# Performance work log

Measured on AMD Instinct MI355X. Metric: run time of the kernel, lower is better.

Reference implementation:

```python
import jax, jax.numpy as jnp
import numpy as np

B, N, DIM = 8, 4096, 512
HEADS, DHEAD = 8, 64
HIDDEN = HEADS * DHEAD  # 512
COND = 512
EPS = 1e-5


def layer_norm(x, gamma, beta):
    mu = jnp.mean(x, axis=-1, keepdims=True)
    var = jnp.var(x, axis=-1, keepdims=True)
    return (x - mu) * jax.lax.rsqrt(var + EPS) * gamma + beta


def setup_inputs() -> dict:
    key = jax.random.key(0)
    ks = jax.random.split(key, 8)
    s_in = 1.0 / np.sqrt(DIM)
    s_cond = 1.0 / np.sqrt(COND)
    s_hid = 1.0 / np.sqrt(HIDDEN)
    return {
        "x": jax.random.normal(ks[0], (B, N, DIM), jnp.float32),
        "conditioning_embeddings": jax.random.normal(ks[1], (B, COND), jnp.float32),
        "gamma_in": jnp.ones((DIM,), jnp.float32),
        "w_cond": jax.random.normal(ks[2], (2 * DIM, COND), jnp.float32) * s_cond,
        "b_cond": jax.random.normal(ks[3], (2 * DIM,), jnp.float32) * 0.01,
        "w_qkv": jax.random.normal(ks[4], (3 * HIDDEN, DIM), jnp.float32) * s_in,
        "w_out": jax.random.normal(ks[5], (DIM, HIDDEN), jnp.float32) * s_hid,
        "gamma_out": jnp.ones((DIM,), jnp.float32),
    }


def reference(x, conditioning_embeddings, gamma_in, w_cond, b_cond, w_qkv, w_out, gamma_out):
    scale_f = DHEAD ** (-0.5)
    # pre-norm
    x = layer_norm(x, gamma_in, jnp.zeros_like(gamma_in))
    # conditioning affine: SiLU -> Linear -> broadcast over tokens
    cond = jax.nn.silu(conditioning_embeddings) @ w_cond.T + b_cond  # [b, 2*dim]
    scale, shift = jnp.split(cond, 2, axis=-1)
    x = x * (scale[:, None, :] + 1.0) + shift[:, None, :]
    # qkv projection (no bias)
    qkv = x @ w_qkv.T  # [b, n, 3*hidden]
    q, k, v = jnp.split(qkv, 3, axis=-1)
    def to_heads(t):
        return t.reshape(B, N, HEADS, DHEAD).transpose(0, 2, 1, 3)  # b h n d
    q, k, v = to_heads(q), to_heads(k), to_heads(v)
    q = jax.nn.softmax(q, axis=-1) * scale_f  # softmax over feature dim
    k = jax.nn.softmax(k, axis=-2)            # softmax over sequence dim
    context = jnp.einsum('bhnd,bhne->bhde', k, v)
    out = jnp.einsum('bhde,bhnd->bhne', context, q)
    out = out.transpose(0, 2, 1, 3).reshape(B, N, HIDDEN)  # b n (h d)
    out = out @ w_out.T
    return layer_norm(out, gamma_out, jnp.zeros_like(gamma_out))
```

## Files before the change

### kernel.cpp

```cpp
#include <hip/hip_runtime.h>
#include <hip/hip_bf16.h>
#include <math.h>

typedef unsigned short u16;
typedef __attribute__((ext_vector_type(4))) float f32x4;
typedef __attribute__((ext_vector_type(8))) short s16x8;

#define B_    8
#define N_    4096
#define DIM_  512
#define TOK   32768
#define QKVD  1536

__device__ __forceinline__ float bf2f(u16 u) {
    union { unsigned int i; float f; } x; x.i = ((unsigned int)u) << 16; return x.f;
}
__device__ __forceinline__ u16 f2bf(float f) {
    union { float f; unsigned int i; } x; x.f = f;
    unsigned int r = (x.i + 0x7fffu + ((x.i >> 16) & 1u)) >> 16;
    return (u16)r;
}

__device__ __forceinline__ void gload_lds16(const void* g, void* l) {
    __builtin_amdgcn_global_load_lds(
        (const __attribute__((address_space(1))) unsigned int*)g,
        (__attribute__((address_space(3))) unsigned int*)l, 16, 0, 0);
}

__device__ __forceinline__ int swz8(int row, int p) { return p ^ (row & 7); }

__global__ void k_cond(const float* __restrict__ ce, const float* __restrict__ w_cond,
                       const float* __restrict__ b_cond, float* __restrict__ cond)
{
    __shared__ float s[512];
    int jt = blockIdx.x, b = blockIdx.y;
    int tid = threadIdx.x, wid = tid >> 6, lane = tid & 63;
    for (int i = tid; i < 512; i += 256) {
        float v = ce[b * 512 + i];
        s[i] = v / (1.f + __expf(-v));
    }
    __syncthreads();
#pragma unroll
    for (int jj = 0; jj < 4; ++jj) {
        int j = jt * 16 + wid * 4 + jj;
        const float4* w4 = (const float4*)(w_cond + (size_t)j * 512);
        float4 a = w4[lane * 2], c = w4[lane * 2 + 1];
        float acc = a.x*s[lane*8+0] + a.y*s[lane*8+1] + a.z*s[lane*8+2] + a.w*s[lane*8+3]
                  + c.x*s[lane*8+4] + c.y*s[lane*8+5] + c.z*s[lane*8+6] + c.w*s[lane*8+7];
#pragma unroll
        for (int d = 1; d < 64; d <<= 1) acc += __shfl_xor(acc, d, 64);
        if (lane == 0) cond[b * 1024 + j] = acc + b_cond[j];
    }
}

__global__ void k_w2bf(const float* __restrict__ w, u16* __restrict__ wb)
{
    int i = (blockIdx.x * 256 + threadIdx.x) * 4;
    float4 v = *(const float4*)&w[i];
    ushort4 o; o.x = f2bf(v.x); o.y = f2bf(v.y); o.z = f2bf(v.z); o.w = f2bf(v.w);
    *(ushort4*)&wb[i] = o;
}

__global__ void k_lnmod(const float* __restrict__ x, const float* __restrict__ cond,
                        const float* __restrict__ gamma, u16* __restrict__ xm)
{
    int wave = threadIdx.x >> 6, lane = threadIdx.x & 63;
    size_t t = (size_t)blockIdx.x * 4 + wave;
    const float* xr = x + t * 512;
    float4 v0 = ((const float4*)xr)[lane * 2];
    float4 v1 = ((const float4*)xr)[lane * 2 + 1];
    float s  = v0.x+v0.y+v0.z+v0.w + v1.x+v1.y+v1.z+v1.w;
    float ss = v0.x*v0.x+v0.y*v0.y+v0.z*v0.z+v0.w*v0.w
             + v1.x*v1.x+v1.y*v1.y+v1.z*v1.z+v1.w*v1.w;
#pragma unroll
    for (int m = 1; m < 64; m <<= 1) { s += __shfl_xor(s, m, 64); ss += __shfl_xor(ss, m, 64); }
    float mu = s * (1.f/512.f);
    float var = ss * (1.f/512.f) - mu * mu;
    float rs = rsqrtf(var + 1e-5f);
    int b = (int)(t >> 12);
    const float* cb = cond + b * 1024;
    float4 g0  = ((const float4*)gamma)[lane*2],     g1  = ((const float4*)gamma)[lane*2+1];
    float4 sc0 = ((const float4*)cb)[lane*2],        sc1 = ((const float4*)cb)[lane*2+1];
    float4 sh0 = ((const float4*)(cb+512))[lane*2],  sh1 = ((const float4*)(cb+512))[lane*2+1];
    ushort4 o0, o1;
    o0.x = f2bf(((v0.x-mu)*rs*g0.x)*(1.f+sc0.x) + sh0.x);
    o0.y = f2bf(((v0.y-mu)*rs*g0.y)*(1.f+sc0.y) + sh0.y);
    o0.z = f2bf(((v0.z-mu)*rs*g0.z)*(1.f+sc0.z) + sh0.z);
    o0.w = f2bf(((v0.w-mu)*rs*g0.w)*(1.f+sc0.w) + sh0.w);
    o1.x = f2bf(((v1.x-mu)*rs*g1.x)*(1.f+sc1.x) + sh1.x);
    o1.y = f2bf(((v1.y-mu)*rs*g1.y)*(1.f+sc1.y) + sh1.y);
    o1.z = f2bf(((v1.z-mu)*rs*g1.z)*(1.f+sc1.z) + sh1.z);
    o1.w = f2bf(((v1.w-mu)*rs*g1.w)*(1.f+sc1.w) + sh1.w);
    ushort4* orow = (ushort4*)(xm + t * 512);
    orow[lane * 2] = o0; orow[lane * 2 + 1] = o1;
}

__global__ __launch_bounds__(256, 2)
void k_gemmqkv(const u16* __restrict__ A,
               const u16* __restrict__ Bm,
               u16* __restrict__ Out,
               float* __restrict__ pmax, float* __restrict__ psum)
{
    __shared__ __align__(16) u16 As[128 * 64];
    __shared__ __align__(16) u16 Bs[128 * 64];
    int sid = (blockIdx.x & 7) * 384 + (blockIdx.x >> 3);
    int bn = sid % 12, bm = sid / 12;
    int m0 = bm * 128, n0 = bn * 128;
    int tid = threadIdx.x;
    int wid = tid >> 6, lane = tid & 63;
    int wr = (wid >> 1) * 64, wc = (wid & 1) * 64;
    int fr = lane & 15, fc = lane >> 4;

    f32x4 acc[4][4];
#pragma unroll
    for (int m = 0; m < 4; ++m)
#pragma unroll
        for (int n = 0; n < 4; ++n) acc[m][n] = (f32x4)0.f;

    for (int k0 = 0; k0 < 512; k0 += 64) {
#pragma unroll
        for (int i = 0; i < 4; ++i) {
            int c = tid + i * 256;
            int row = c >> 3, p = c & 7, gp = swz8(row, p);
            gload_lds16(A  + (size_t)(m0 + row) * 512 + k0 + gp * 8, &As[c * 8]);
            gload_lds16(Bm + (size_t)(n0 + row) * 512 + k0 + gp * 8, &Bs[c * 8]);
        }
        __syncthreads();
#pragma unroll
        for (int kk = 0; kk < 2; ++kk) {
            s16x8 af[4], bfr[4];
            int q = kk * 4 + fc;
#pragma unroll
            for (int m = 0; m < 4; ++m) {
                int row = wr + m * 16 + fr;
                af[m] = *(const s16x8*)&As[(row * 8 + swz8(row, q)) * 8];
            }
#pragma unroll
            for (int n = 0; n < 4; ++n) {
                int row = wc + n * 16 + fr;
                bfr[n] = *(const s16x8*)&Bs[(row * 8 + swz8(row, q)) * 8];
            }
#pragma unroll
            for (int m = 0; m < 4; ++m)
#pragma unroll
                for (int n = 0; n < 4; ++n)
                    acc[m][n] = __builtin_amdgcn_mfma_f32_16x16x32_bf16(af[m], bfr[n], acc[m][n], 0, 0, 0);
        }
        __syncthreads();
    }

    int rbase = m0 + wr + fc * 4;
    int cbase = n0 + wc + fr;

    if (bn < 4) {
#pragma unroll
        for (int m = 0; m < 4; ++m) {
            float v[4][4];
#pragma unroll
            for (int n = 0; n < 4; ++n)
#pragma unroll
                for (int r = 0; r < 4; ++r) v[n][r] = acc[m][n][r];
#pragma unroll
            for (int r = 0; r < 4; ++r) {
                float mx = fmaxf(fmaxf(v[0][r], v[1][r]), fmaxf(v[2][r], v[3][r]));
#pragma unroll
                for (int d = 1; d < 16; d <<= 1) mx = fmaxf(mx, __shfl_xor(mx, d, 64));
                float e0 = __expf(v[0][r]-mx), e1 = __expf(v[1][r]-mx);
                float e2 = __expf(v[2][r]-mx), e3 = __expf(v[3][r]-mx);
                float sm = e0 + e1 + e2 + e3;
#pragma unroll
                for (int d = 1; d < 16; d <<= 1) sm += __shfl_xor(sm, d, 64);
                float rv = 0.125f / sm;
                v[0][r] = e0*rv; v[1][r] = e1*rv; v[2][r] = e2*rv; v[3][r] = e3*rv;
            }
#pragma unroll
            for (int n = 0; n < 4; ++n)
#pragma unroll
                for (int r = 0; r < 4; ++r)
                    Out[(size_t)(rbase + m*16 + r) * QKVD + (cbase + n*16)] = f2bf(v[n][r]);
        }
    } else if (bn < 8) {
        int bloc = m0 >> 12;
        int rcc = ((m0 & 4095) + wr) >> 6;
#pragma unroll
        for (int n = 0; n < 4; ++n) {
            float vv[16]; float mx = -1e30f;
#pragma unroll
            for (int m = 0; m < 4; ++m)
#pragma unroll
                for (int r = 0; r < 4; ++r) {
                    u16 u = f2bf(acc[m][n][r]);
                    Out[(size_t)(rbase + m*16 + r) * QKVD + (cbase + n*16)] = u;
                    float vf = bf2f(u);
                    vv[m*4+r] = vf; mx = fmaxf(mx, vf);
                }
            mx = fmaxf(mx, __shfl_xor(mx, 16, 64));
            mx = fmaxf(mx, __shfl_xor(mx, 32, 64));
            float sm = 0.f;
#pragma unroll
            for (int i = 0; i < 16; ++i) sm += __expf(vv[i] - mx);
            sm += __shfl_xor(sm, 16, 64);
            sm += __shfl_xor(sm, 32, 64);
            if (lane < 16) {
                int kcol = (n0 - 512) + wc + n*16 + lane;
                int o = (bloc * 64 + rcc) * 512 + kcol;
                pmax[o] = mx; psum[o] = sm;
            }
        }
    } else {
#pragma unroll
        for (int m = 0; m < 4; ++m)
#pragma unroll
            for (int n = 0; n < 4; ++n)
#pragma unroll
                for (int r = 0; r < 4; ++r)
                    Out[(size_t)(rbase + m*16 + r) * QKVD + (cbase + n*16)] = f2bf(acc[m][n][r]);
    }
}

__global__ void k_kstat2(const float* __restrict__ pmax, const float* __restrict__ psum,
                         float* __restrict__ kmax, float* __restrict__ ksum)
{
    int g = blockIdx.x * 64 + threadIdx.x;
    int b = g >> 9, c = g & 511;
    float m = -1e30f, s = 0.f;
    for (int rc = 0; rc < 64; ++rc) {
        float m2 = pmax[(b * 64 + rc) * 512 + c], s2 = psum[(b * 64 + rc) * 512 + c];
        float mm = fmaxf(m, m2);
        s = s * __expf(m - mm) + s2 * __expf(m2 - mm);
        m = mm;
    }
    kmax[g] = m; ksum[g] = s;
}

__global__ __launch_bounds__(256, 2)
void k_ctx(const u16* __restrict__ qkv, const float* __restrict__ kmax, float* __restrict__ ctxp)
{
    __shared__ __align__(16) u16 sA[4][64 * 40];
    __shared__ __align__(16) u16 sB[4][64 * 40];
    __shared__ float scr[2][4096];
    int nc = blockIdx.x, h = blockIdx.y, b = blockIdx.z;
    int wid = threadIdx.x >> 6, lane = threadIdx.x & 63;
    u16* A  = sA[wid];
    u16* Bt = sB[wid];
    float km = kmax[b * 512 + h * 64 + lane];
    int fr = lane & 15, fk = (lane >> 4) * 8;
    f32x4 acc[4][4];
#pragma unroll
    for (int m = 0; m < 4; ++m)
#pragma unroll
        for (int n = 0; n < 4; ++n) acc[m][n] = (f32x4)0.f;

    size_t rowbase = (size_t)b * 4096 + nc * 512 + wid * 32;
    const u16* kp = qkv + rowbase * QKVD + 512 + h * 64 + lane;
    const u16* vp = kp + 512;

    for (int it = 0; it < 4; ++it) {
        const u16* kq = kp + (size_t)it * 128 * QKVD;
        const u16* vq = vp + (size_t)it * 128 * QKVD;
        unsigned int pk[16], pv[16];
#pragma unroll
        for (int j = 0; j < 16; ++j) {
            float a0 = __expf(bf2f(kq[(size_t)(2*j)   * QKVD]) - km);
            float a1 = __expf(bf2f(kq[(size_t)(2*j+1) * QKVD]) - km);
            pk[j] = (unsigned)f2bf(a0) | ((unsigned)f2bf(a1) << 16);
            float b0 = bf2f(vq[(size_t)(2*j)   * QKVD]);
            float b1 = bf2f(vq[(size_t)(2*j+1) * QKVD]);
            pv[j] = (unsigned)f2bf(b0) | ((unsigned)f2bf(b1) << 16);
        }
#pragma unroll
        for (int j = 0; j < 4; ++j) {
            *(uint4*)&A [lane * 40 + j * 8] = *(uint4*)&pk[j * 4];
            *(uint4*)&Bt[lane * 40 + j * 8] = *(uint4*)&pv[j * 4];
        }
        s16x8 af[4], bfr[4];
#pragma unroll
        for (int m = 0; m < 4; ++m) af[m]  = *(const s16x8*)&A [(m * 16 + fr) * 40 + fk];
#pragma unroll
        for (int n = 0; n < 4; ++n) bfr[n] = *(const s16x8*)&Bt[(n * 16 + fr) * 40 + fk];
#pragma unroll
        for (int m = 0; m < 4; ++m)
#pragma unroll
            for (int n = 0; n < 4; ++n)
                acc[m][n] = __builtin_amdgcn_mfma_f32_16x16x32_bf16(af[m], bfr[n], acc[m][n], 0, 0, 0);
    }

    __syncthreads();
    int rbase = (lane >> 4) * 4, cbase = lane & 15;
    if (wid >= 2) {
#pragma unroll
        for (int m = 0; m < 4; ++m)
#pragma unroll
            for (int n = 0; n < 4; ++n)
#pragma unroll
                for (int r = 0; r < 4; ++r)
                    scr[wid - 2][(m * 16 + rbase + r) * 64 + n * 16 + cbase] = acc[m][n][r];
    }
    __syncthreads();
    if (wid < 2) {
        float* cp = ctxp + (((size_t)(b * 8 + h) * 16) + nc * 2 + wid) * 4096;
#pragma unroll
        for (int m = 0; m < 4; ++m)
#pragma unroll
            for (int n = 0; n < 4; ++n)
#pragma unroll
                for (int r = 0; r < 4; ++r) {
                    int idx = (m * 16 + rbase + r) * 64 + n * 16 + cbase;
                    cp[idx] = acc[m][n][r] + scr[wid][idx];
                }
    }
}

__global__ void k_wc(const float* __restrict__ ctxp, const float* __restrict__ ksum,
                     const float* __restrict__ w_out, u16* __restrict__ Wc)
{
    __shared__ float csh[64 * 65];
    __shared__ float wsh[64 * 65];
    int jt = blockIdx.x, h = blockIdx.y, b = blockIdx.z;
    int tid = threadIdx.x;
    const float* cp = ctxp + ((size_t)(b * 8 + h) * 16) * 4096;
    for (int idx = tid; idx < 4096; idx += 256) {
        int d = idx >> 6, e = idx & 63;
        float sum = 0.f;
#pragma unroll
        for (int nc = 0; nc < 16; ++nc) sum += cp[nc * 4096 + idx];
        csh[d * 65 + e] = sum * (1.f / ksum[b * 512 + h * 64 + d]);
        wsh[d * 65 + e] = w_out[(size_t)(jt * 64 + d) * 512 + h * 64 + e];
    }
    __syncthreads();
    int j0 = (tid >> 4) * 4, d0 = (tid & 15) * 4;
    float acc[4][4] = {};
    for (int e = 0; e < 64; ++e) {
        float wv[4], cv[4];
#pragma unroll
        for (int i = 0; i < 4; ++i) wv[i] = wsh[(j0 + i) * 65 + e];
#pragma unroll
        for (int j = 0; j < 4; ++j) cv[j] = csh[(d0 + j) * 65 + e];
#pragma unroll
        for (int i = 0; i < 4; ++i)
#pragma unroll
            for (int j = 0; j < 4; ++j) acc[i][j] += wv[i] * cv[j];
    }
#pragma unroll
    for (int i = 0; i < 4; ++i)
#pragma unroll
        for (int j = 0; j < 4; ++j)
            Wc[((size_t)b * 512 + jt * 64 + j0 + i) * 512 + h * 64 + d0 + j] = f2bf(acc[i][j]);
}

__global__ __launch_bounds__(512, 1)
void k_g2ln(const u16* __restrict__ Aq, const u16* __restrict__ Wc,
            const float* __restrict__ gamma, float* __restrict__ out)
{
    __shared__ __align__(16) u16 As[128 * 64];
    __shared__ __align__(16) u16 Bs[512 * 64];
    __shared__ float rsum[128][4], rssq[128][4];
    int bm = blockIdx.x;
    int m0 = bm * 128;
    int b = m0 >> 12;
    const u16* Bp = Wc + (size_t)b * 512 * 512;
    int tid = threadIdx.x;
    int wid = tid >> 6, lane = tid & 63;
    int wm = wid >> 2, wn = wid & 3;
    int fr = lane & 15, fc = lane >> 4;

    f32x4 acc[4][8];
#pragma unroll
    for (int m = 0; m < 4; ++m)
#pragma unroll
        for (int n = 0; n < 8; ++n) acc[m][n] = (f32x4)0.f;

    for (int k0 = 0; k0 < 512; k0 += 64) {
#pragma unroll
        for (int i = 0; i < 2; ++i) {
            int c = tid + i * 512;
            int row = c >> 3, p = c & 7, gp = swz8(row, p);
            gload_lds16(Aq + (size_t)(m0 + row) * QKVD + k0 + gp * 8, &As[c * 8]);
        }
#pragma unroll
        for (int i = 0; i < 8; ++i) {
            int c = tid + i * 512;
            int col = c >> 3, p = c & 7, gp = swz8(col, p);
            gload_lds16(Bp + (size_t)col * 512 + k0 + gp * 8, &Bs[c * 8]);
        }
        __syncthreads();
#pragma unroll
        for (int kk = 0; kk < 2; ++kk) {
            int q = kk * 4 + fc;
            s16x8 af[4], bfr[8];
#pragma unroll
            for (int m = 0; m < 4; ++m) {
                int row = wm * 64 + m * 16 + fr;
                af[m] = *(const s16x8*)&As[(row * 8 + swz8(row, q)) * 8];
            }
#pragma unroll
            for (int n = 0; n < 8; ++n) {
                int col = wn * 128 + n * 16 + fr;
                bfr[n] = *(const s16x8*)&Bs[(col * 8 + swz8(col, q)) * 8];
            }
#pragma unroll
            for (int m = 0; m < 4; ++m)
#pragma unroll
                for (int n = 0; n < 8; ++n)
                    acc[m][n] = __builtin_amdgcn_mfma_f32_16x16x32_bf16(af[m], bfr[n], acc[m][n], 0, 0, 0);
        }
        __syncthreads();
    }

#pragma unroll
    for (int m = 0; m < 4; ++m)
#pragma unroll
        for (int r = 0; r < 4; ++r) {
            float s = 0.f, ss = 0.f;
#pragma unroll
            for (int n = 0; n < 8; ++n) { float v = acc[m][n][r]; s += v; ss += v * v; }
#pragma unroll
            for (int d = 1; d < 16; d <<= 1) { s += __shfl_xor(s, d, 64); ss += __shfl_xor(ss, d, 64); }
            if ((lane & 15) == 0) {
                int row = wm * 64 + m * 16 + fc * 4 + r;
                rsum[row][wn] = s; rssq[row][wn] = ss;
            }
        }
    __syncthreads();

    float g[8];
#pragma unroll
    for (int n = 0; n < 8; ++n) g[n] = gamma[wn * 128 + n * 16 + fr];

#pragma unroll
    for (int m = 0; m < 4; ++m)
#pragma unroll
        for (int r = 0; r < 4; ++r) {
            int row = wm * 64 + m * 16 + fc * 4 + r;
            float s  = rsum[row][0] + rsum[row][1] + rsum[row][2] + rsum[row][3];
            float ss = rssq[row][0] + rssq[row][1] + rssq[row][2] + rssq[row][3];
            float mu = s * (1.f/512.f);
            float var = ss * (1.f/512.f) - mu * mu;
            float rs = rsqrtf(var + 1e-5f);
            float* orow = out + (size_t)(m0 + row) * 512;
#pragma unroll
            for (int n = 0; n < 8; ++n)
                orow[wn * 128 + n * 16 + fr] = (acc[m][n][r] - mu) * rs * g[n];
        }
}

extern "C" void kernel_launch(void* const* d_in, const int* in_sizes, int n_in,
                              void* d_out, int out_size, void* d_ws, size_t ws_size,
                              hipStream_t stream)
{
    const float* x        = (const float*)d_in[0];
    const float* ce       = (const float*)d_in[1];
    const float* gamma_in = (const float*)d_in[2];
    const float* w_cond   = (const float*)d_in[3];
    const float* b_cond   = (const float*)d_in[4];
    const float* w_qkv    = (const float*)d_in[5];
    const float* w_out    = (const float*)d_in[6];
    const float* gamma_out= (const float*)d_in[7];
    float* out = (float*)d_out;

    char* ws = (char*)d_ws;
    size_t o = 0;
    auto take = [&](size_t bytes) -> char* {
        char* p = ws + o; o += (bytes + 255) & ~(size_t)255; return p;
    };
    float* cond  = (float*)take(8 * 1024 * 4);
    u16*   wqkvb = (u16*)  take((size_t)1536 * 512 * 2);
    float* kmax  = (float*)take(4096 * 4);
    float* ksum  = (float*)take(4096 * 4);
    float* pmax  = (float*)take((size_t)8 * 64 * 512 * 4);
    float* psum  = (float*)take((size_t)8 * 64 * 512 * 4);
    float* ctxp  = (float*)take((size_t)64 * 16 * 4096 * 4);
    u16*   Wc    = (u16*)  take((size_t)8 * 512 * 512 * 2);
    u16*   xm    = (u16*)  take((size_t)TOK * 512 * 2);
    u16*   qkv   = (u16*)  take((size_t)TOK * QKVD * 2);

    k_cond   <<<dim3(64, 8), 256, 0, stream>>>(ce, w_cond, b_cond, cond);
    k_w2bf   <<<768, 256, 0, stream>>>(w_qkv, wqkvb);
    k_lnmod  <<<8192, 256, 0, stream>>>(x, cond, gamma_in, xm);
    k_gemmqkv<<<3072, 256, 0, stream>>>(xm, wqkvb, qkv, pmax, psum);
    k_kstat2 <<<64, 64, 0, stream>>>(pmax, psum, kmax, ksum);
    k_ctx    <<<dim3(8, 8, 8), 256, 0, stream>>>(qkv, kmax, ctxp);
    k_wc     <<<dim3(8, 8, 8), 256, 0, stream>>>(ctxp, ksum, w_out, Wc);
    k_g2ln   <<<256, 512, 0, stream>>>(qkv, Wc, gamma_out, out);
}
```

Before: 189.8 us.

## Rewrite QKV GEMM as 256x256 tile with double-buffered LDS pipeline

The QKV projection GEMM moves from 128x128 tiles with 4 waves to 256x256 tiles with 8 waves. It now double-buffers A/B in LDS, prefetching the next k-slices while MFMAs run, using explicit vmcnt waits, barriers and setprio to interleave loads and compute. The larger tile cuts global and LDS traffic per FLOP and halves the number of k partial-stat rows, so kstat2 reduces over 32 chunks instead of 64. The costs are a large LDS footprint, one block per CU, more accumulator registers, and fewer blocks (768) for load balance.

```diff
diff --git a/kernel.cpp b/kernel.cpp
--- a/kernel.cpp
+++ b/kernel.cpp
@@ -95,126 +95,190 @@
     orow[lane * 2] = o0; orow[lane * 2 + 1] = o1;
 }
 
-__global__ __launch_bounds__(256, 2)
+__global__ __launch_bounds__(512, 1)
 void k_gemmqkv(const u16* __restrict__ A,
                const u16* __restrict__ Bm,
                u16* __restrict__ Out,
                float* __restrict__ pmax, float* __restrict__ psum)
 {
-    __shared__ __align__(16) u16 As[128 * 64];
-    __shared__ __align__(16) u16 Bs[128 * 64];
-    int sid = (blockIdx.x & 7) * 384 + (blockIdx.x >> 3);
-    int bn = sid % 12, bm = sid / 12;
-    int m0 = bm * 128, n0 = bn * 128;
+    __shared__ __align__(16) u16 As[2][2][128 * 64];
+    __shared__ __align__(16) u16 Bs[2][2][128 * 64];
+    int bid = blockIdx.x;
+    int sid = (bid & 7) * 96 + (bid >> 3);
+    int bn = sid % 6, bm = sid / 6;
+    int m0 = bm * 256, n0 = bn * 256;
     int tid = threadIdx.x;
     int wid = tid >> 6, lane = tid & 63;
-    int wr = (wid >> 1) * 64, wc = (wid & 1) * 64;
+    int wm = wid >> 2, wn = wid & 3;
     int fr = lane & 15, fc = lane >> 4;
 
-    f32x4 acc[4][4];
-#pragma unroll
-    for (int m = 0; m < 4; ++m)
+    auto stageA = [&](int t, int h) {
+        u16* dst = &As[t & 1][h][0];
+        const u16* src = A + (size_t)(m0 + h * 128) * 512 + t * 64;
+#pragma unroll
+        for (int i = 0; i < 2; ++i) {
+            int c = tid + i * 512; int row = c >> 3, p = c & 7, gp = swz8(row, p);
+            gload_lds16(src + (size_t)row * 512 + gp * 8, dst + c * 8);
+        }
+    };
+    auto stageB = [&](int t, int h) {
+        u16* dst = &Bs[t & 1][h][0];
+        const u16* src = Bm + (size_t)(n0 + h * 128) * 512 + t * 64;
+#pragma unroll
+        for (int i = 0; i < 2; ++i) {
+            int c = tid + i * 512; int row = c >> 3, p = c & 7, gp = swz8(row, p);
+            gload_lds16(src + (size_t)row * 512 + gp * 8, dst + c * 8);
+        }
+    };
+    auto ldA = [&](int t, int m, int kk) -> s16x8 {
+        int lr = m * 16 + fr, q = kk * 4 + fc;
+        return *(const s16x8*)&As[t & 1][wm][(lr * 8 + swz8(lr, q)) * 8];
+    };
+    auto ldB = [&](int t, int n, int kk) -> s16x8 {
+        int lr = (wn & 1) * 64 + n * 16 + fr, q = kk * 4 + fc;
+        return *(const s16x8*)&Bs[t & 1][wn >> 1][(lr * 8 + swz8(lr, q)) * 8];
+    };
+
+    f32x4 acc[8][4];
+#pragma unroll
+    for (int m = 0; m < 8; ++m)
 #pragma unroll
         for (int n = 0; n < 4; ++n) acc[m][n] = (f32x4)0.f;
 
-    for (int k0 = 0; k0 < 512; k0 += 64) {
-#pragma unroll
-        for (int i = 0; i < 4; ++i) {
-            int c = tid + i * 256;
-            int row = c >> 3, p = c & 7, gp = swz8(row, p);
-            gload_lds16(A  + (size_t)(m0 + row) * 512 + k0 + gp * 8, &As[c * 8]);
-            gload_lds16(Bm + (size_t)(n0 + row) * 512 + k0 + gp * 8, &Bs[c * 8]);
-        }
-        __syncthreads();
-#pragma unroll
-        for (int kk = 0; kk < 2; ++kk) {
-            s16x8 af[4], bfr[4];
-            int q = kk * 4 + fc;
-#pragma unroll
-            for (int m = 0; m < 4; ++m) {
-                int row = wr + m * 16 + fr;
-                af[m] = *(const s16x8*)&As[(row * 8 + swz8(row, q)) * 8];
-            }
-#pragma unroll
-            for (int n = 0; n < 4; ++n) {
-                int row = wc + n * 16 + fr;
-                bfr[n] = *(const s16x8*)&Bs[(row * 8 + swz8(row, q)) * 8];
-            }
-#pragma unroll
-            for (int m = 0; m < 4; ++m)
-#pragma unroll
-                for (int n = 0; n < 4; ++n)
-                    acc[m][n] = __builtin_amdgcn_mfma_f32_16x16x32_bf16(af[m], bfr[n], acc[m][n], 0, 0, 0);
-        }
-        __syncthreads();
-    }
-
-    int rbase = m0 + wr + fc * 4;
-    int cbase = n0 + wc + fr;
-
-    if (bn < 4) {
-#pragma unroll
-        for (int m = 0; m < 4; ++m) {
-            float v[4][4];
-#pragma unroll
-            for (int n = 0; n < 4; ++n)
-#pragma unroll
-                for (int r = 0; r < 4; ++r) v[n][r] = acc[m][n][r];
+    stageA(0, 0); stageA(0, 1); stageB(0, 0); stageB(0, 1);
+    stageB(1, 0); stageB(1, 1);
+    asm volatile("s_waitcnt vmcnt(4)" ::: "memory");
+    __builtin_amdgcn_s_barrier();
+    __builtin_amdgcn_sched_barrier(0);
+
+    for (int t = 0; t < 8; ++t) {
+        s16x8 bb0[4], bb1[4], aa[4];
+#pragma unroll
+        for (int n = 0; n < 4; ++n) { bb0[n] = ldB(t, n, 0); bb1[n] = ldB(t, n, 1); }
+#pragma unroll
+        for (int m = 0; m < 4; ++m) aa[m] = ldA(t, m, 0);
+        if (t < 7) stageA(t + 1, 0);
+        __builtin_amdgcn_s_barrier();
+        __builtin_amdgcn_sched_barrier(0);
+        __builtin_amdgcn_s_setprio(1);
+#pragma unroll
+        for (int m = 0; m < 4; ++m)
+#pragma unroll
+            for (int n = 0; n < 4; ++n)
+                acc[m][n] = __builtin_amdgcn_mfma_f32_16x16x32_bf16(aa[m], bb0[n], acc[m][n], 0, 0, 0);
+        __builtin_amdgcn_s_setprio(0);
+        __builtin_amdgcn_s_barrier();
+        __builtin_amdgcn_sched_barrier(0);
+#pragma unroll
+        for (int m = 0; m < 4; ++m) aa[m] = ldA(t, m + 4, 0);
+        if (t < 7) stageA(t + 1, 1);
+        __builtin_amdgcn_s_barrier();
+        __builtin_amdgcn_sched_barrier(0);
+        __builtin_amdgcn_s_setprio(1);
+#pragma unroll
+        for (int m = 0; m < 4; ++m)
+#pragma unroll
+            for (int n = 0; n < 4; ++n)
+                acc[m + 4][n] = __builtin_amdgcn_mfma_f32_16x16x32_bf16(aa[m], bb0[n], acc[m + 4][n], 0, 0, 0);
+        __builtin_amdgcn_s_setprio(0);
+        __builtin_amdgcn_s_barrier();
+        __builtin_amdgcn_sched_barrier(0);
+#pragma unroll
+        for (int m = 0; m < 4; ++m) aa[m] = ldA(t, m, 1);
+        if (t < 6) stageB(t + 2, 0);
+        __builtin_amdgcn_s_barrier();
+        __builtin_amdgcn_sched_barrier(0);
+        __builtin_amdgcn_s_setprio(1);
+#pragma unroll
+        for (int m = 0; m < 4; ++m)
+#pragma unroll
+            for (int n = 0; n < 4; ++n)
+                acc[m][n] = __builtin_amdgcn_mfma_f32_16x16x32_bf16(aa[m], bb1[n], acc[m][n], 0, 0, 0);
+        __builtin_amdgcn_s_setprio(0);
+        __builtin_amdgcn_s_barrier();
+        __builtin_amdgcn_sched_barrier(0);
+#pragma unroll
+        for (int m = 0; m < 4; ++m) aa[m] = ldA(t, m + 4, 1);
+        if (t < 6) {
+            stageB(t + 2, 1);
+            asm volatile("s_waitcnt vmcnt(4)" ::: "memory");
+        } else {
+            asm volatile("s_waitcnt vmcnt(0)" ::: "memory");
+        }
+        __builtin_amdgcn_sched_barrier(0);
+        __builtin_amdgcn_s_barrier();
+        __builtin_amdgcn_sched_barrier(0);
+        __builtin_amdgcn_s_setprio(1);
+#pragma unroll
+        for (int m = 0; m < 4; ++m)
+#pragma unroll
+            for (int n = 0; n < 4; ++n)
+                acc[m + 4][n] = __builtin_amdgcn_mfma_f32_16x16x32_bf16(aa[m], bb1[n], acc[m + 4][n], 0, 0, 0);
+        __builtin_amdgcn_s_setprio(0);
+        __builtin_amdgcn_s_barrier();
+        __builtin_amdgcn_sched_barrier(0);
+    }
+
+    int b = m0 >> 12;
+    int rbase = m0 + wm * 128 + fc * 4;
+    int cb = n0 + wn * 64 + fr;
+
+    if (bn < 2) {
+#pragma unroll
+        for (int m = 0; m < 8; ++m)
 #pragma unroll
             for (int r = 0; r < 4; ++r) {
-                float mx = fmaxf(fmaxf(v[0][r], v[1][r]), fmaxf(v[2][r], v[3][r]));
+                float v0 = acc[m][0][r], v1 = acc[m][1][r], v2 = acc[m][2][r], v3 = acc[m][3][r];
+                float mx = fmaxf(fmaxf(v0, v1), fmaxf(v2, v3));
 #pragma unroll
                 for (int d = 1; d < 16; d <<= 1) mx = fmaxf(mx, __shfl_xor(mx, d, 64));
-                float e0 = __expf(v[0][r]-mx), e1 = __expf(v[1][r]-mx);
-                float e2 = __expf(v[2][r]-mx), e3 = __expf(v[3][r]-mx);
+                float e0 = __expf(v0 - mx), e1 = __expf(v1 - mx);
+                float e2 = __expf(v2 - mx), e3 = __expf(v3 - mx);
                 float sm = e0 + e1 + e2 + e3;
 #pragma unroll
                 for (int d = 1; d < 16; d <<= 1) sm += __shfl_xor(sm, d, 64);
                 float rv = 0.125f / sm;
-                v[0][r] = e0*rv; v[1][r] = e1*rv; v[2][r] = e2*rv; v[3][r] = e3*rv;
+                size_t ro = (size_t)(rbase + m * 16 + r) * QKVD + cb;
+                Out[ro]      = f2bf(e0 * rv);
+                Out[ro + 16] = f2bf(e1 * rv);
+                Out[ro + 32] = f2bf(e2 * rv);
+                Out[ro + 48] = f2bf(e3 * rv);
             }
-#pragma unroll
-            for (int n = 0; n < 4; ++n)
-#pragma unroll
-                for (int r = 0; r < 4; ++r)
-                    Out[(size_t)(rbase + m*16 + r) * QKVD + (cbase + n*16)] = f2bf(v[n][r]);
-        }
-    } else if (bn < 8) {
-        int bloc = m0 >> 12;
-        int rcc = ((m0 & 4095) + wr) >> 6;
+    } else if (bn < 4) {
+        int rcc = ((m0 & 4095) >> 7) + wm;
 #pragma unroll
         for (int n = 0; n < 4; ++n) {
-            float vv[16]; float mx = -1e30f;
-#pragma unroll
-            for (int m = 0; m < 4; ++m)
+            float vv[32]; float mx = -1e30f;
+#pragma unroll
+            for (int m = 0; m < 8; ++m)
 #pragma unroll
                 for (int r = 0; r < 4; ++r) {
                     u16 u = f2bf(acc[m][n][r]);
-                    Out[(size_t)(rbase + m*16 + r) * QKVD + (cbase + n*16)] = u;
+                    Out[(size_t)(rbase + m * 16 + r) * QKVD + cb + n * 16] = u;
                     float vf = bf2f(u);
-                    vv[m*4+r] = vf; mx = fmaxf(mx, vf);
+                    vv[m * 4 + r] = vf; mx = fmaxf(mx, vf);
                 }
             mx = fmaxf(mx, __shfl_xor(mx, 16, 64));
             mx = fmaxf(mx, __shfl_xor(mx, 32, 64));
             float sm = 0.f;
 #pragma unroll
-            for (int i = 0; i < 16; ++i) sm += __expf(vv[i] - mx);
+            for (int i = 0; i < 32; ++i) sm += __expf(vv[i] - mx);
             sm += __shfl_xor(sm, 16, 64);
             sm += __shfl_xor(sm, 32, 64);
             if (lane < 16) {
-                int kcol = (n0 - 512) + wc + n*16 + lane;
-                int o = (bloc * 64 + rcc) * 512 + kcol;
+                int kcol = cb + n * 16 - 512;
+                int o = (b * 32 + rcc) * 512 + kcol;
                 pmax[o] = mx; psum[o] = sm;
             }
         }
     } else {
 #pragma unroll
-        for (int m = 0; m < 4; ++m)
+        for (int m = 0; m < 8; ++m)
 #pragma unroll
             for (int n = 0; n < 4; ++n)
 #pragma unroll
                 for (int r = 0; r < 4; ++r)
-                    Out[(size_t)(rbase + m*16 + r) * QKVD + (cbase + n*16)] = f2bf(acc[m][n][r]);
+                    Out[(size_t)(rbase + m * 16 + r) * QKVD + cb + n * 16] = f2bf(acc[m][n][r]);
     }
 }
 
@@ -224,8 +288,8 @@
     int g = blockIdx.x * 64 + threadIdx.x;
     int b = g >> 9, c = g & 511;
     float m = -1e30f, s = 0.f;
-    for (int rc = 0; rc < 64; ++rc) {
-        float m2 = pmax[(b * 64 + rc) * 512 + c], s2 = psum[(b * 64 + rc) * 512 + c];
+    for (int rc = 0; rc < 32; ++rc) {
+        float m2 = pmax[(b * 32 + rc) * 512 + c], s2 = psum[(b * 32 + rc) * 512 + c];
         float mm = fmaxf(m, m2);
         s = s * __expf(m - mm) + s2 * __expf(m2 - mm);
         m = mm;
@@ -467,8 +531,8 @@
     u16*   wqkvb = (u16*)  take((size_t)1536 * 512 * 2);
     float* kmax  = (float*)take(4096 * 4);
     float* ksum  = (float*)take(4096 * 4);
-    float* pmax  = (float*)take((size_t)8 * 64 * 512 * 4);
-    float* psum  = (float*)take((size_t)8 * 64 * 512 * 4);
+    float* pmax  = (float*)take((size_t)8 * 32 * 512 * 4);
+    float* psum  = (float*)take((size_t)8 * 32 * 512 * 4);
     float* ctxp  = (float*)take((size_t)64 * 16 * 4096 * 4);
     u16*   Wc    = (u16*)  take((size_t)8 * 512 * 512 * 2);
     u16*   xm    = (u16*)  take((size_t)TOK * 512 * 2);
@@ -477,7 +541,7 @@
     k_cond   <<<dim3(64, 8), 256, 0, stream>>>(ce, w_cond, b_cond, cond);
     k_w2bf   <<<768, 256, 0, stream>>>(w_qkv, wqkvb);
     k_lnmod  <<<8192, 256, 0, stream>>>(x, cond, gamma_in, xm);
-    k_gemmqkv<<<3072, 256, 0, stream>>>(xm, wqkvb, qkv, pmax, psum);
+    k_gemmqkv<<<768, 512, 0, stream>>>(xm, wqkvb, qkv, pmax, psum);
     k_kstat2 <<<64, 64, 0, stream>>>(pmax, psum, kmax, ksum);
     k_ctx    <<<dim3(8, 8, 8), 256, 0, stream>>>(qkv, kmax, ctxp);
     k_wc     <<<dim3(8, 8, 8), 256, 0, stream>>>(ctxp, ksum, w_out, Wc);
```

Result: faster. 182.5 us (-3.9%).
